# Kernel tuning notes

Measured on AMD Instinct MI355X. Metric: run time of the kernel, lower is better.

The kernel has to match this reference:

```python
import jax, jax.numpy as jnp
import numpy as np

WINDOW_SIZE = 11
SIGMA = 1.5
C1 = 0.01 ** 2
C2 = 0.03 ** 2


def _gaussian_window(channels):
    coords = jnp.arange(WINDOW_SIZE, dtype=jnp.float32) - WINDOW_SIZE // 2
    g = jnp.exp(-coords ** 2 / (2.0 * SIGMA ** 2))
    g = g / g.sum()
    w2d = g[:, None] * g[None, :]                      # [K, K]
    # depthwise kernel: [out_ch=C, in_ch/groups=1, K, K]
    return jnp.broadcast_to(w2d[None, None], (channels, 1, WINDOW_SIZE, WINDOW_SIZE))


def _depthwise_conv(x, window):
    # x: [B, C, H, W]; grouped conv with feature_group_count = C, SAME padding
    C = x.shape[1]
    pad = WINDOW_SIZE // 2
    return jax.lax.conv_general_dilated(
        x, window,
        window_strides=(1, 1),
        padding=((pad, pad), (pad, pad)),
        dimension_numbers=("NCHW", "OIHW", "NCHW"),
        feature_group_count=C,
    )


def setup_inputs() -> dict:
    key = jax.random.key(0)
    k1, k2 = jax.random.split(key)
    shape = (16, 3, 512, 512)
    pred = jax.random.uniform(k1, shape, dtype=jnp.float32)
    target = jax.random.uniform(k2, shape, dtype=jnp.float32)
    return {"pred": pred, "target": target}


def reference(pred, target):
    C = pred.shape[1]
    window = _gaussian_window(C)
    mu_p = _depthwise_conv(pred, window)
    mu_t = _depthwise_conv(target, window)
    mu_p_sq = mu_p ** 2
    mu_t_sq = mu_t ** 2
    mu_cross = mu_p * mu_t
    sigma_p_sq = _depthwise_conv(pred ** 2, window) - mu_p_sq
    sigma_t_sq = _depthwise_conv(target ** 2, window) - mu_t_sq
    sigma_cross = _depthwise_conv(pred * target, window) - mu_cross
    ssim_map = ((2.0 * mu_cross + C1) * (2.0 * sigma_cross + C2)) / (
        (mu_p_sq + mu_t_sq + C1) * (sigma_p_sq + sigma_t_sq + C2)
    )
    return 1.0 - ssim_map.mean()
```

## Files before the change

### kernel.cpp

```cpp
#include <hip/hip_runtime.h>

#define HH 512
#define WW 512
#define NPLANE 48
#define BY 128
#define BX 128
#define CHK 16
#define RING 32
#define PSTR 40
#define KS 11

typedef __attribute__((ext_vector_type(8))) short short8;
typedef __attribute__((ext_vector_type(4))) float floatx4;
typedef __attribute__((ext_vector_type(2))) float float2v;
typedef __attribute__((ext_vector_type(2))) __bf16 bf16x2v;

__device__ inline unsigned pk2bf_rne(float a, float b) {
    union { float f; unsigned u; } ua, ub;
    ua.f = a; ub.f = b;
    unsigned lo = (ua.u + 0x7FFFu + ((ua.u >> 16) & 1u)) >> 16;
    unsigned hi = (ub.u + 0x7FFFu + ((ub.u >> 16) & 1u)) >> 16;
    return lo | (hi << 16);
}

__device__ inline unsigned pkbf2(float2v f) {
    bf16x2v v = __builtin_convertvector(f, bf16x2v);
    return __builtin_bit_cast(unsigned, v);
}

struct Raw   { float4 p0, p1, t0, t1; };
struct Frags { short8 p, t, q, pt; };

__global__ __launch_bounds__(256, 4) void ssim_kernel(
    const float* __restrict__ pred, const float* __restrict__ target,
    float* __restrict__ ws_sum)
{
    __shared__ __align__(16) short ring[4][2][4][16][PSTR];
    __shared__ float red[4];

    const int tid = threadIdx.x;
    const int wv = tid >> 6;
    const int lane = tid & 63;
    const int m = lane & 15;
    const int quad = lane >> 4;

    float wsum = 0.f;
#pragma unroll
    for (int k = 0; k < KS; ++k) {
        float d = (float)(k - 5);
        wsum += __expf(-d * d * (1.0f / 4.5f));
    }
    const float invs = 1.0f / wsum;

    short8 Wf;
    {
        union { short8 v; unsigned u[4]; } W;
#pragma unroll
        for (int jj = 0; jj < 4; ++jj) {
            float v0, v1;
            {
                int idx = quad * 8 + 2 * jj - m - 3;
                float d = (float)(idx - 5);
                v0 = (idx >= 0 && idx < KS) ? __expf(-d * d * (1.0f / 4.5f)) * invs : 0.f;
            }
            {
                int idx = quad * 8 + 2 * jj + 1 - m - 3;
                float d = (float)(idx - 5);
                v1 = (idx >= 0 && idx < KS) ? __expf(-d * d * (1.0f / 4.5f)) * invs : 0.f;
            }
            W.u[jj] = pk2bf_rne(v0, v1);
        }
        Wf = W.v;
    }

    const size_t poff = (size_t)blockIdx.z * HH * WW;
    const int Y0 = blockIdx.y * BY;

    const int XA = blockIdx.x * BX + wv * 16;
    const int cA = XA - 8 + quad * 8;
    const int cB = cA + 64;
    const bool okA0 = (unsigned)cA < (unsigned)WW;
    const bool okA1 = (unsigned)(cA + 4) < (unsigned)WW;
    const bool okB0 = (unsigned)cB < (unsigned)WW;
    const bool okB1 = (unsigned)(cB + 4) < (unsigned)WW;
    const float* __restrict__ pcA = pred + poff + cA;
    const float* __restrict__ tcA = target + poff + cA;
    const float* __restrict__ pcB = pred + poff + cB;
    const float* __restrict__ tcB = target + poff + cB;

    const float2v C1v = {1.0e-4f, 1.0e-4f};
    const float2v C2v = {9.0e-4f, 9.0e-4f};
    float lsum = 0.f;
    const floatx4 z = {0.f, 0.f, 0.f, 0.f};

    auto load_raw = [&](const float* __restrict__ pc, const float* __restrict__ tc,
                        bool ok0, bool ok1, int k) -> Raw {
        Raw r;
        r.p0 = make_float4(0, 0, 0, 0); r.p1 = make_float4(0, 0, 0, 0);
        r.t0 = make_float4(0, 0, 0, 0); r.t1 = make_float4(0, 0, 0, 0);
        const int row = Y0 + CHK * k - 8 + m;
        if ((unsigned)row < (unsigned)HH) {
            const float* pr = pc + (size_t)row * WW;
            const float* tr = tc + (size_t)row * WW;
            if (ok0) { r.p0 = *(const float4*)pr;       r.t0 = *(const float4*)tr; }
            if (ok1) { r.p1 = *(const float4*)(pr + 4); r.t1 = *(const float4*)(tr + 4); }
        }
        return r;
    };

    auto h_step = [&](int pipe, const Raw& r, int sb) {
        const float2v pa[4] = {{r.p0.x, r.p0.y}, {r.p0.z, r.p0.w},
                               {r.p1.x, r.p1.y}, {r.p1.z, r.p1.w}};
        const float2v tb[4] = {{r.t0.x, r.t0.y}, {r.t0.z, r.t0.w},
                               {r.t1.x, r.t1.y}, {r.t1.z, r.t1.w}};
        union { short8 v; unsigned u[4]; } Fp, Ft, Fq, Fpt;
#pragma unroll
        for (int jj = 0; jj < 4; ++jj) {
            Fp.u[jj]  = pkbf2(pa[jj]);
            Ft.u[jj]  = pkbf2(tb[jj]);
            Fq.u[jj]  = pkbf2(pa[jj] * pa[jj] + tb[jj] * tb[jj]);
            Fpt.u[jj] = pkbf2(pa[jj] * tb[jj]);
        }
        floatx4 Dp  = __builtin_amdgcn_mfma_f32_16x16x32_bf16(Fp.v,  Wf, z, 0, 0, 0);
        floatx4 Dt  = __builtin_amdgcn_mfma_f32_16x16x32_bf16(Ft.v,  Wf, z, 0, 0, 0);
        floatx4 Dq  = __builtin_amdgcn_mfma_f32_16x16x32_bf16(Fq.v,  Wf, z, 0, 0, 0);
        floatx4 Dpt = __builtin_amdgcn_mfma_f32_16x16x32_bf16(Fpt.v, Wf, z, 0, 0, 0);
        const int slot = (sb + quad * 4) & (RING - 1);
        uint2 v;
        v.x = pkbf2(float2v{Dp[0],  Dp[1]});  v.y = pkbf2(float2v{Dp[2],  Dp[3]});
        *(uint2*)&ring[wv][pipe][0][m][slot] = v;
        v.x = pkbf2(float2v{Dt[0],  Dt[1]});  v.y = pkbf2(float2v{Dt[2],  Dt[3]});
        *(uint2*)&ring[wv][pipe][1][m][slot] = v;
        v.x = pkbf2(float2v{Dq[0],  Dq[1]});  v.y = pkbf2(float2v{Dq[2],  Dq[3]});
        *(uint2*)&ring[wv][pipe][2][m][slot] = v;
        v.x = pkbf2(float2v{Dpt[0], Dpt[1]}); v.y = pkbf2(float2v{Dpt[2], Dpt[3]});
        *(uint2*)&ring[wv][pipe][3][m][slot] = v;
    };

    auto vread = [&](int pipe, int base) -> Frags {
        const int sq = (base + quad * 8) & (RING - 1);
        Frags f;
        f.p  = *(const short8*)&ring[wv][pipe][0][m][sq];
        f.t  = *(const short8*)&ring[wv][pipe][1][m][sq];
        f.q  = *(const short8*)&ring[wv][pipe][2][m][sq];
        f.pt = *(const short8*)&ring[wv][pipe][3][m][sq];
        return f;
    };

    auto vfin = [&](const Frags& f) {
        floatx4 Mp  = __builtin_amdgcn_mfma_f32_16x16x32_bf16(Wf, f.p,  z, 0, 0, 0);
        floatx4 Mt  = __builtin_amdgcn_mfma_f32_16x16x32_bf16(Wf, f.t,  z, 0, 0, 0);
        floatx4 Mq  = __builtin_amdgcn_mfma_f32_16x16x32_bf16(Wf, f.q,  z, 0, 0, 0);
        floatx4 Mpt = __builtin_amdgcn_mfma_f32_16x16x32_bf16(Wf, f.pt, z, 0, 0, 0);
#pragma unroll
        for (int h = 0; h < 2; ++h) {
            const float2v mup = {Mp[2*h],  Mp[2*h+1]};
            const float2v mut = {Mt[2*h],  Mt[2*h+1]};
            const float2v mq  = {Mq[2*h],  Mq[2*h+1]};
            const float2v mpt = {Mpt[2*h], Mpt[2*h+1]};
            const float2v mupsq = mup * mup, mutsq = mut * mut, mucr = mup * mut;
            const float2v scr = mpt - mucr;
            const float2v n1 = mucr + mucr + C1v;
            const float2v n2 = scr + scr + C2v;
            const float2v d1 = mupsq + mutsq + C1v;
            const float2v d2 = (mq - mupsq - mutsq) + C2v;
            const float2v num = n1 * n2, den = d1 * d2;
            lsum += __fdividef(num[0], den[0]) + __fdividef(num[1], den[1]);
        }
    };

    Raw CA, CB;
    CA = load_raw(pcA, tcA, okA0, okA1, 0);
    CB = load_raw(pcB, tcB, okB0, okB1, 0);
    h_step(0, CA, 24); h_step(1, CB, 24);
    CA = load_raw(pcA, tcA, okA0, okA1, 1);
    CB = load_raw(pcB, tcB, okB0, okB1, 1);
    h_step(0, CA, 8);  h_step(1, CB, 8);
    CA = load_raw(pcA, tcA, okA0, okA1, 2);
    CB = load_raw(pcB, tcB, okB0, okB1, 2);

#pragma unroll 1
    for (int ii = 0; ii < 6; ii += 2) {
        {
            Frags FA = vread(0, 24), FB = vread(1, 24);
            h_step(0, CA, 24);
            h_step(1, CB, 24);
            CA = load_raw(pcA, tcA, okA0, okA1, ii + 3);
            CB = load_raw(pcB, tcB, okB0, okB1, ii + 3);
            vfin(FA); vfin(FB);
        }
        {
            Frags FA = vread(0, 8), FB = vread(1, 8);
            h_step(0, CA, 8);
            h_step(1, CB, 8);
            CA = load_raw(pcA, tcA, okA0, okA1, ii + 4);
            CB = load_raw(pcB, tcB, okB0, okB1, ii + 4);
            vfin(FA); vfin(FB);
        }
    }
    {
        Frags FA = vread(0, 24), FB = vread(1, 24);
        h_step(0, CA, 24);
        h_step(1, CB, 24);
        vfin(FA); vfin(FB);
    }
    {
        Frags FA = vread(0, 8), FB = vread(1, 8);
        vfin(FA); vfin(FB);
    }

#pragma unroll
    for (int off = 32; off > 0; off >>= 1) lsum += __shfl_down(lsum, off, 64);
    if (lane == 0) red[wv] = lsum;
    __syncthreads();
    if (tid == 0) {
        atomicAdd(ws_sum, red[0] + red[1] + red[2] + red[3]);
    }
}

__global__ void finalize_kernel(const float* __restrict__ ws_sum,
                                float* __restrict__ out) {
    out[0] = 1.0f - ws_sum[0] * (1.0f / 12582912.0f);
}

extern "C" void kernel_launch(void* const* d_in, const int* in_sizes, int n_in,
                              void* d_out, int out_size, void* d_ws, size_t ws_size,
                              hipStream_t stream) {
    const float* pred = (const float*)d_in[0];
    const float* target = (const float*)d_in[1];
    float* out = (float*)d_out;
    float* ws = (float*)d_ws;

    hipMemsetAsync(ws, 0, sizeof(float), stream);
    dim3 grid(WW / BX, HH / BY, NPLANE);
    ssim_kernel<<<grid, 256, 0, stream>>>(pred, target, ws);
    finalize_kernel<<<1, 1, 0, stream>>>(ws, out);
}
```

Measured before the change: 144.6 us.

## Swizzle block order across XCDs and interleave the two column halves per step

Block IDs are remapped so that blocks landing on the same XCD (round-robin by ID mod 8) cover contiguous tiles. The intent is that neighbouring tiles, which share halo rows and columns, hit the same L2. The main loop now fully processes half A (vread, h_step, prefetch, vfin) before starting half B. This shortens live ranges, lowers register pressure and spreads LDS and global traffic more evenly. The block-reduction scratch array is dropped and the ring buffer is reused, which saves a small amount of LDS but depends on each wave touching only its own ring slice at the end.

Measured after the change: 147.7 us. +2.1%, slower.

```diff
diff --git a/kernel.cpp b/kernel.cpp
--- a/kernel.cpp
+++ b/kernel.cpp
@@ -36,13 +36,18 @@
     float* __restrict__ ws_sum)
 {
     __shared__ __align__(16) short ring[4][2][4][16][PSTR];
-    __shared__ float red[4];
 
     const int tid = threadIdx.x;
     const int wv = tid >> 6;
     const int lane = tid & 63;
     const int m = lane & 15;
     const int quad = lane >> 4;
+
+    const int lid = blockIdx.x + 4 * blockIdx.y + 16 * blockIdx.z;
+    const int swz = (lid & 7) * 96 + (lid >> 3);
+    const int bx = swz & 3;
+    const int by = (swz >> 2) & 3;
+    const int bz = swz >> 4;
 
     float wsum = 0.f;
 #pragma unroll
@@ -73,10 +78,10 @@
         Wf = W.v;
     }
 
-    const size_t poff = (size_t)blockIdx.z * HH * WW;
-    const int Y0 = blockIdx.y * BY;
-
-    const int XA = blockIdx.x * BX + wv * 16;
+    const size_t poff = (size_t)bz * HH * WW;
+    const int Y0 = by * BY;
+
+    const int XA = bx * BX + wv * 16;
     const int cA = XA - 8 + quad * 8;
     const int cB = cA + 64;
     const bool okA0 = (unsigned)cA < (unsigned)WW;
@@ -182,39 +187,50 @@
 #pragma unroll 1
     for (int ii = 0; ii < 6; ii += 2) {
         {
-            Frags FA = vread(0, 24), FB = vread(1, 24);
+            Frags FA = vread(0, 24);
             h_step(0, CA, 24);
+            CA = load_raw(pcA, tcA, okA0, okA1, ii + 3);
+            vfin(FA);
+            Frags FB = vread(1, 24);
             h_step(1, CB, 24);
-            CA = load_raw(pcA, tcA, okA0, okA1, ii + 3);
             CB = load_raw(pcB, tcB, okB0, okB1, ii + 3);
-            vfin(FA); vfin(FB);
+            vfin(FB);
         }
         {
-            Frags FA = vread(0, 8), FB = vread(1, 8);
+            Frags FA = vread(0, 8);
             h_step(0, CA, 8);
+            CA = load_raw(pcA, tcA, okA0, okA1, ii + 4);
+            vfin(FA);
+            Frags FB = vread(1, 8);
             h_step(1, CB, 8);
-            CA = load_raw(pcA, tcA, okA0, okA1, ii + 4);
             CB = load_raw(pcB, tcB, okB0, okB1, ii + 4);
-            vfin(FA); vfin(FB);
+            vfin(FB);
         }
     }
     {
-        Frags FA = vread(0, 24), FB = vread(1, 24);
+        Frags FA = vread(0, 24);
         h_step(0, CA, 24);
+        vfin(FA);
+        Frags FB = vread(1, 24);
         h_step(1, CB, 24);
-        vfin(FA); vfin(FB);
+        vfin(FB);
     }
     {
-        Frags FA = vread(0, 8), FB = vread(1, 8);
-        vfin(FA); vfin(FB);
+        Frags FA = vread(0, 8);
+        vfin(FA);
+        Frags FB = vread(1, 8);
+        vfin(FB);
     }
 
 #pragma unroll
     for (int off = 32; off > 0; off >>= 1) lsum += __shfl_down(lsum, off, 64);
-    if (lane == 0) red[wv] = lsum;
+    if (lane == 0) *(float*)&ring[wv][0][0][0][0] = lsum;
     __syncthreads();
     if (tid == 0) {
-        atomicAdd(ws_sum, red[0] + red[1] + red[2] + red[3]);
+        atomicAdd(ws_sum, *(const float*)&ring[0][0][0][0][0]
+                        + *(const float*)&ring[1][0][0][0][0]
+                        + *(const float*)&ring[2][0][0][0][0]
+                        + *(const float*)&ring[3][0][0][0][0]);
     }
 }
 
```
